# Performance work log

Measured on AMD Instinct MI355X. Metric: run time of the kernel, lower is better.

The kernel has to match this reference:

```python
import jax, jax.numpy as jnp
import numpy as np

B, T, E, H = 8, 4096, 1024, 128

def setup_inputs() -> dict:
    key = jax.random.key(0)
    kx, kq, kk, kv = jax.random.split(key, 4)
    x = jax.random.normal(kx, (B, T, E), dtype=jnp.float32)
    # bias-free Linear weights stored as (in, out) for x @ W
    scale = 1.0 / np.sqrt(E)
    Wq = jax.random.normal(kq, (E, H), dtype=jnp.float32) * scale
    Wk = jax.random.normal(kk, (E, H), dtype=jnp.float32) * scale
    Wv = jax.random.normal(kv, (E, H), dtype=jnp.float32) * scale
    return {"x": x, "Wq": Wq, "Wk": Wk, "Wv": Wv}

def reference(x, Wq, Wk, Wv):
    # x: (B,T,E) -> out: (B,T,H). Causal single-head attention, dropout p=0 (no-op).
    q = x @ Wq  # (B,T,H)
    k = x @ Wk
    v = x @ Wv
    head_norm = jnp.sqrt(jnp.float32(q.shape[-1]))
    att = jnp.einsum('bth,bsh->bts', q, k) / head_norm  # (B,T,T)
    causal = jnp.tril(jnp.ones((x.shape[1], x.shape[1]), dtype=bool))
    att = jnp.where(causal, att, -jnp.inf)
    att = jax.nn.softmax(att, axis=-1)
    return jnp.einsum('bts,bsh->bth', att, v)
```

## Files before the change

### kernel.cpp

```cpp
#include <hip/hip_runtime.h>
#include <hip/hip_bf16.h>
#include <stdint.h>

#define Bn 8
#define Tn 4096
#define En 1024
#define Hn 128
#define SCALE 0.08838834764831845f

typedef __attribute__((ext_vector_type(8))) short bf16x8;
typedef __attribute__((ext_vector_type(4))) float f32x4;

__device__ __forceinline__ float bf2f(unsigned short v) {
    return __uint_as_float(((unsigned int)v) << 16);
}
__device__ __forceinline__ unsigned int pkbf(float a, float b) {
    __hip_bfloat162 h = __float22bfloat162_rn(make_float2(a, b));
    union { __hip_bfloat162 h2; unsigned int u; } cv;
    cv.h2 = h;
    return cv.u;
}

__device__ __forceinline__ void gll16(const unsigned short* g, unsigned short* l) {
    __builtin_amdgcn_global_load_lds(
        (const __attribute__((address_space(1))) void*)g,
        (__attribute__((address_space(3))) void*)l, 16, 0, 0);
}

__global__ __launch_bounds__(256)
void xcvt(const float* __restrict__ x, unsigned short* __restrict__ xb) {
    const size_t i = ((size_t)blockIdx.x * 256 + threadIdx.x) * 16;
    const float4* src = (const float4*)(x + i);
    float4 a = src[0], b = src[1], c = src[2], d = src[3];
    uint4 o0, o1;
    o0.x = pkbf(a.x, a.y); o0.y = pkbf(a.z, a.w);
    o0.z = pkbf(b.x, b.y); o0.w = pkbf(b.z, b.w);
    o1.x = pkbf(c.x, c.y); o1.y = pkbf(c.z, c.w);
    o1.z = pkbf(d.x, d.y); o1.w = pkbf(d.z, d.w);
    *(uint4*)(xb + i) = o0;
    *(uint4*)(xb + i + 8) = o1;
}

__global__ __launch_bounds__(256)
void wcvt(const float* __restrict__ Wq, const float* __restrict__ Wk,
          const float* __restrict__ Wv, unsigned short* __restrict__ wt3) {
    const int which = blockIdx.x;
    const int k0 = blockIdx.y * 128;
    const float* W = (which == 0) ? Wq : (which == 1) ? Wk : Wv;
    unsigned short* wt = wt3 + (size_t)which * 131072;

    __shared__ unsigned short wl[128 * 132];
    const int t = threadIdx.x;
#pragma unroll
    for (int i = 0; i < 16; ++i) {
        const int idx = t + i * 256;
        const int k = idx >> 5, c4 = idx & 31;
        float4 v = *(const float4*)&W[(size_t)(k0 + k) * Hn + c4 * 4];
        uint2 p;
        p.x = pkbf(v.x, v.y);
        p.y = pkbf(v.z, v.w);
        *(uint2*)&wl[k * 132 + c4 * 4] = p;
    }
    __syncthreads();
#pragma unroll
    for (int j = 0; j < 32; ++j) {
        const int idx = t + j * 256;
        const int n = idx >> 6, kp = idx & 63;
        unsigned int u = (unsigned int)wl[(2 * kp) * 132 + n] |
                         ((unsigned int)wl[(2 * kp + 1) * 132 + n] << 16);
        *(unsigned int*)&wt[(size_t)n * 1024 + k0 + 2 * kp] = u;
    }
}

#define QSWZ(r, c) (((r) << 7) + ((c) ^ (((r) & 7) << 4)))

__global__ __launch_bounds__(256)
void qkv2(const unsigned short* __restrict__ xb,
          const unsigned short* __restrict__ wt3,
          unsigned short* __restrict__ Qo,
          unsigned short* __restrict__ Ko,
          unsigned short* __restrict__ Vo) {
    const int mt = blockIdx.x;
    const int which = blockIdx.y;
    const unsigned short* wt = wt3 + (size_t)which * 131072;
    unsigned short* out = (which == 0) ? Qo : (which == 1) ? Ko : Vo;
    const float scale = (which == 0) ? SCALE : 1.0f;

    __shared__ alignas(16) unsigned short Xs[2][128 * 64];
    __shared__ alignas(16) unsigned short Ws[2][128 * 64];

    const int t = threadIdx.x;
    const int w = t >> 6;
    const int lane = t & 63;
    const int quad = lane >> 4;
    const int l16 = lane & 15;
    const int r8 = lane >> 3;
    const int cb = lane & 7;

    const unsigned short* xtile = xb + (size_t)(mt * 128) * En;

    f32x4 acc[2][8];
#pragma unroll
    for (int mi = 0; mi < 2; ++mi)
#pragma unroll
        for (int nst = 0; nst < 8; ++nst) acc[mi][nst] = (f32x4){0.f, 0.f, 0.f, 0.f};

    auto stage = [&](int buf, int kt) {
#pragma unroll
        for (int i = 0; i < 4; ++i) {
            const int row = i * 32 + w * 8 + r8;
            gll16(xtile + (size_t)row * En + kt * 64 + ((cb ^ (row & 7)) * 8),
                  &Xs[buf][(i * 32 + w * 8) * 64]);
        }
#pragma unroll
        for (int i = 0; i < 4; ++i) {
            const int row = i * 32 + w * 8 + r8;
            gll16(wt + (size_t)row * 1024 + kt * 64 + ((cb ^ (row & 7)) * 8),
                  &Ws[buf][(i * 32 + w * 8) * 64]);
        }
    };

    stage(0, 0);
    __syncthreads();

    for (int kt = 0; kt < 16; ++kt) {
        const int buf = kt & 1;
        if (kt < 15) stage(buf ^ 1, kt + 1);
        const char* xs = (const char*)Xs[buf];
        const char* ws = (const char*)Ws[buf];
#pragma unroll
        for (int ks = 0; ks < 2; ++ks) {
            bf16x8 af[2];
#pragma unroll
            for (int mi = 0; mi < 2; ++mi)
                af[mi] = *(const bf16x8*)(xs + QSWZ(w * 32 + mi * 16 + l16, ks * 64 + quad * 16));
#pragma unroll
            for (int nst = 0; nst < 8; ++nst) {
                bf16x8 bfr = *(const bf16x8*)(ws + QSWZ(nst * 16 + l16, ks * 64 + quad * 16));
                acc[0][nst] = __builtin_amdgcn_mfma_f32_16x16x32_bf16(bfr, af[0], acc[0][nst], 0, 0, 0);
                acc[1][nst] = __builtin_amdgcn_mfma_f32_16x16x32_bf16(bfr, af[1], acc[1][nst], 0, 0, 0);
            }
        }
        if (kt < 15) __syncthreads();
    }

#pragma unroll
    for (int mi = 0; mi < 2; ++mi) {
        const size_t rowbase = (size_t)(mt * 128 + w * 32 + mi * 16 + l16) * Hn;
#pragma unroll
        for (int nst = 0; nst < 8; ++nst) {
            f32x4 v = acc[mi][nst];
            uint2 pk;
            pk.x = pkbf(v[0] * scale, v[1] * scale);
            pk.y = pkbf(v[2] * scale, v[3] * scale);
            *(uint2*)(out + rowbase + nst * 16 + quad * 4) = pk;
        }
    }
}

__global__ __launch_bounds__(256)
void qkv_mfma(const float* __restrict__ x,
              const float* __restrict__ Wq,
              const float* __restrict__ Wk,
              const float* __restrict__ Wv,
              unsigned short* __restrict__ Qo,
              unsigned short* __restrict__ Ko,
              unsigned short* __restrict__ Vo) {
    const int mt = blockIdx.x;
    const int which = blockIdx.y;
    const float* W = (which == 0) ? Wq : (which == 1) ? Wk : Wv;
    unsigned short* out = (which == 0) ? Qo : (which == 1) ? Ko : Vo;
    const float scale = (which == 0) ? SCALE : 1.0f;

    __shared__ alignas(16) unsigned short Xs[128 * 72];
    __shared__ alignas(16) unsigned short Wt[128 * 72];

    const int t = threadIdx.x;
    const int w = t >> 6;
    const int lane = t & 63;
    const int quad = lane >> 4;
    const int l16 = lane & 15;

    const int xrow = t >> 1;
    const int xkc = (t & 1) * 32;
    const int ws0 = (t & 31) * 2;
    const int wd0 = (t >> 5) * 16;

    const float* xsrc0 = x + (size_t)(mt * 128 + xrow) * En + xkc;

    f32x4 acc[2][8];
#pragma unroll
    for (int mi = 0; mi < 2; ++mi)
#pragma unroll
        for (int nst = 0; nst < 8; ++nst) acc[mi][nst] = (f32x4){0.f, 0.f, 0.f, 0.f};

    float4 xpre[8], wpre[8];
    {
        const float* src = xsrc0;
#pragma unroll
        for (int i = 0; i < 8; ++i) xpre[i] = *(const float4*)(src + i * 4);
        const float* w0 = W + (size_t)ws0 * Hn + wd0;
        const float* w1 = w0 + Hn;
#pragma unroll
        for (int i = 0; i < 4; ++i) wpre[i] = *(const float4*)(w0 + i * 4);
#pragma unroll
        for (int i = 0; i < 4; ++i) wpre[4 + i] = *(const float4*)(w1 + i * 4);
    }

    for (int kt = 0; kt < 16; ++kt) {
        __syncthreads();
        {
            unsigned int u[16];
#pragma unroll
            for (int i = 0; i < 8; ++i) {
                u[2 * i]     = pkbf(xpre[i].x, xpre[i].y);
                u[2 * i + 1] = pkbf(xpre[i].z, xpre[i].w);
            }
#pragma unroll
            for (int i = 0; i < 4; ++i)
                *(uint4*)&Xs[xrow * 72 + xkc + i * 8] = ((const uint4*)u)[i];

            const float* ax = (const float*)&wpre[0];
            const float* bx = (const float*)&wpre[4];
#pragma unroll
            for (int dd = 0; dd < 16; ++dd)
                *(unsigned int*)&Wt[(wd0 + dd) * 72 + ws0] = pkbf(ax[dd], bx[dd]);
        }
        if (kt < 15) {
            const float* src = xsrc0 + (kt + 1) * 64;
#pragma unroll
            for (int i = 0; i < 8; ++i) xpre[i] = *(const float4*)(src + i * 4);
            const float* w0 = W + (size_t)((kt + 1) * 64 + ws0) * Hn + wd0;
            const float* w1 = w0 + Hn;
#pragma unroll
            for (int i = 0; i < 4; ++i) wpre[i] = *(const float4*)(w0 + i * 4);
#pragma unroll
            for (int i = 0; i < 4; ++i) wpre[4 + i] = *(const float4*)(w1 + i * 4);
        }
        __syncthreads();

#pragma unroll
        for (int ks = 0; ks < 2; ++ks) {
            bf16x8 af[2];
#pragma unroll
            for (int mi = 0; mi < 2; ++mi)
                af[mi] = *(const bf16x8*)&Xs[(w * 32 + mi * 16 + l16) * 72 + ks * 32 + quad * 8];
#pragma unroll
            for (int nst = 0; nst < 8; ++nst) {
                bf16x8 bfr = *(const bf16x8*)&Wt[(nst * 16 + l16) * 72 + ks * 32 + quad * 8];
                acc[0][nst] = __builtin_amdgcn_mfma_f32_16x16x32_bf16(bfr, af[0], acc[0][nst], 0, 0, 0);
                acc[1][nst] = __builtin_amdgcn_mfma_f32_16x16x32_bf16(bfr, af[1], acc[1][nst], 0, 0, 0);
            }
        }
    }

#pragma unroll
    for (int mi = 0; mi < 2; ++mi) {
        const size_t rowbase = (size_t)(mt * 128 + w * 32 + mi * 16 + l16) * Hn;
#pragma unroll
        for (int nst = 0; nst < 8; ++nst) {
            f32x4 v = acc[mi][nst];
            uint2 pk;
            pk.x = pkbf(v[0] * scale, v[1] * scale);
            pk.y = pkbf(v[2] * scale, v[3] * scale);
            *(uint2*)(out + rowbase + nst * 16 + quad * 4) = pk;
        }
    }
}

#define KSWZ(r, c) (((r) << 8) + ((c) ^ (((r) & 7) << 4)))
#define VSWZ(r, c) (((r) << 7) + ((c) ^ (((r) & 7) << 4)))

__global__ __launch_bounds__(256, 2)
void flash_mfma(const unsigned short* __restrict__ Qb,
                const unsigned short* __restrict__ Kb,
                const unsigned short* __restrict__ Vb,
                float* __restrict__ out) {
    const int b = blockIdx.x;
    const int bx = blockIdx.y;
    const int qt = (bx < 32) ? (63 - bx) : (bx - 32);
    const int t = threadIdx.x;
    const int w = t >> 6;
    const int g = w >> 1;
    const int rg = w & 1;
    const int lane = t & 63;
    const int quad = lane >> 4;
    const int l16 = lane & 15;
    const int t128 = t & 127;

    extern __shared__ unsigned short pool[];
    char* const poolb = (char*)pool;
    char* const Kg = poolb + g * 16384;
    char* const Vg = poolb + 32768 + g * 16384;
    char* const Pw = poolb + 65536 + w * 4096;
    float* const Os = (float*)poolb;
    float* const Ex = (float*)(poolb + 40960);
    float* const Em = (float*)(poolb + 73728);
    float* const El = Em + 64;

    const size_t gbase = (size_t)b * ((size_t)Tn * Hn);
    const unsigned short* kbase = Kb + gbase;
    const unsigned short* vbase = Vb + gbase;

    const int l_hi = lane >> 4;
    const int cpr = (lane & 15) * 16;
    const int vs0 = (t128 & 31) * 2;
    const int vd0 = (t128 >> 5) * 32;

    uint4 va0, va1, va2, va3, vb0, vb1, vb2, vb3;
    if (g <= qt) {
        const unsigned short* vsrc = vbase + (size_t)(g * 64) * Hn;
        va0 = *(const uint4*)&vsrc[vs0 * 128 + vd0];
        va1 = *(const uint4*)&vsrc[vs0 * 128 + vd0 + 8];
        va2 = *(const uint4*)&vsrc[vs0 * 128 + vd0 + 16];
        va3 = *(const uint4*)&vsrc[vs0 * 128 + vd0 + 24];
        vb0 = *(const uint4*)&vsrc[(vs0 + 1) * 128 + vd0];
        vb1 = *(const uint4*)&vsrc[(vs0 + 1) * 128 + vd0 + 8];
        vb2 = *(const uint4*)&vsrc[(vs0 + 1) * 128 + vd0 + 16];
        vb3 = *(const uint4*)&vsrc[(vs0 + 1) * 128 + vd0 + 24];
    }

    {
        const unsigned short* qsrc = Qb + gbase + (size_t)(qt * 64) * Hn;
#pragma unroll
        for (int i = 0; i < 4; ++i) {
            const int row = w * 16 + i * 4 + l_hi;
            const int scol = cpr ^ ((row & 7) << 4);
            gll16(qsrc + row * 128 + (scol >> 1),
                  (unsigned short*)(poolb + w * 4096 + i * 1024));
        }
    }
    __syncthreads();

    bf16x8 qf[2][4];
#pragma unroll
    for (int s = 0; s < 2; ++s)
#pragma unroll
        for (int ks = 0; ks < 4; ++ks)
            qf[s][ks] = *(const bf16x8*)(poolb + KSWZ(rg * 32 + s * 16 + l16, ks * 64 + quad * 16));

    f32x4 acc_o[2][8];
#pragma unroll
    for (int s = 0; s < 2; ++s)
#pragma unroll
        for (int i = 0; i < 8; ++i) acc_o[s][i] = (f32x4){0.f, 0.f, 0.f, 0.f};
    float m_run[2] = {-1e30f, -1e30f};
    float l_run[2] = {0.f, 0.f};

    const int n = (qt >> 1) + 1;
    for (int it = 0; it < n; ++it) {
        const int kt = 2 * it + g;
        const bool active = (kt <= qt);
        __syncthreads();
        if (active) {
            const unsigned short* ktile = kbase + (size_t)(kt * 64) * Hn;
#pragma unroll
            for (int i = 0; i < 8; ++i) {
                const int row = rg * 32 + i * 4 + l_hi;
                const int scol = cpr ^ ((row & 7) << 4);
                gll16(ktile + row * 128 + (scol >> 1),
                      (unsigned short*)(Kg + rg * 8192 + i * 1024));
            }
            const unsigned short* pa0 = (const unsigned short*)&va0;
            const unsigned short* pa1 = (const unsigned short*)&va1;
            const unsigned short* pa2 = (const unsigned short*)&va2;
            const unsigned short* pa3 = (const unsigned short*)&va3;
            const unsigned short* pb0 = (const unsigned short*)&vb0;
            const unsigned short* pb1 = (const unsigned short*)&vb1;
            const unsigned short* pb2 = (const unsigned short*)&vb2;
            const unsigned short* pb3 = (const unsigned short*)&vb3;
#pragma unroll
            for (int dd = 0; dd < 8; ++dd)
                *(unsigned int*)(Vg + VSWZ(vd0 + dd, vs0 * 2)) =
                    (unsigned int)pa0[dd] | ((unsigned int)pb0[dd] << 16);
#pragma unroll
            for (int dd = 0; dd < 8; ++dd)
                *(unsigned int*)(Vg + VSWZ(vd0 + 8 + dd, vs0 * 2)) =
                    (unsigned int)pa1[dd] | ((unsigned int)pb1[dd] << 16);
#pragma unroll
            for (int dd = 0; dd < 8; ++dd)
                *(unsigned int*)(Vg + VSWZ(vd0 + 16 + dd, vs0 * 2)) =
                    (unsigned int)pa2[dd] | ((unsigned int)pb2[dd] << 16);
#pragma unroll
            for (int dd = 0; dd < 8; ++dd)
                *(unsigned int*)(Vg + VSWZ(vd0 + 24 + dd, vs0 * 2)) =
                    (unsigned int)pa3[dd] | ((unsigned int)pb3[dd] << 16);
        }
        __syncthreads();
        if (kt + 2 <= qt) {
            const unsigned short* vsrc = vbase + (size_t)((kt + 2) * 64) * Hn;
            va0 = *(const uint4*)&vsrc[vs0 * 128 + vd0];
            va1 = *(const uint4*)&vsrc[vs0 * 128 + vd0 + 8];
            va2 = *(const uint4*)&vsrc[vs0 * 128 + vd0 + 16];
            va3 = *(const uint4*)&vsrc[vs0 * 128 + vd0 + 24];
            vb0 = *(const uint4*)&vsrc[(vs0 + 1) * 128 + vd0];
            vb1 = *(const uint4*)&vsrc[(vs0 + 1) * 128 + vd0 + 8];
            vb2 = *(const uint4*)&vsrc[(vs0 + 1) * 128 + vd0 + 16];
            vb3 = *(const uint4*)&vsrc[(vs0 + 1) * 128 + vd0 + 24];
        }
        if (!active) continue;

        const bool diag = (kt == qt);
        f32x4 sa[2][4];
#pragma unroll
        for (int st = 0; st < 4; ++st) {
            const bool skipAll = diag && (st > rg * 2 + 1);
            bf16x8 kf[4];
            if (!skipAll) {
#pragma unroll
                for (int ks = 0; ks < 4; ++ks)
                    kf[ks] = *(const bf16x8*)(Kg + KSWZ(st * 16 + l16, ks * 64 + quad * 16));
            }
#pragma unroll
            for (int s = 0; s < 2; ++s) {
                const int qs = rg * 2 + s;
                if (diag && st > qs) {
                    sa[s][st] = (f32x4){-1e30f, -1e30f, -1e30f, -1e30f};
                } else {
                    f32x4 c = (f32x4){0.f, 0.f, 0.f, 0.f};
#pragma unroll
                    for (int ks = 0; ks < 4; ++ks)
                        c = __builtin_amdgcn_mfma_f32_16x16x32_bf16(kf[ks], qf[s][ks], c, 0, 0, 0);
                    if (diag && st == qs) {
#pragma unroll
                        for (int r = 0; r < 4; ++r)
                            if (quad * 4 + r > l16) c[r] = -1e30f;
                    }
                    sa[s][st] = c;
                }
            }
        }

#pragma unroll
        for (int s = 0; s < 2; ++s) {
            float mloc = -1e30f;
#pragma unroll
            for (int st = 0; st < 4; ++st)
#pragma unroll
                for (int r = 0; r < 4; ++r) mloc = fmaxf(mloc, sa[s][st][r]);
            mloc = fmaxf(mloc, __shfl_xor(mloc, 16));
            mloc = fmaxf(mloc, __shfl_xor(mloc, 32));
            const float m_new = fmaxf(m_run[s], mloc);
            const float alpha = __expf(m_run[s] - m_new);
            float lsum = 0.f;
#pragma unroll
            for (int st = 0; st < 4; ++st)
#pragma unroll
                for (int r = 0; r < 4; ++r) {
                    const float e = __expf(sa[s][st][r] - m_new);
                    sa[s][st][r] = e;
                    lsum += e;
                }
            lsum += __shfl_xor(lsum, 16);
            lsum += __shfl_xor(lsum, 32);
            l_run[s] = l_run[s] * alpha + lsum;
            m_run[s] = m_new;
#pragma unroll
            for (int i = 0; i < 8; ++i) acc_o[s][i] *= alpha;
#pragma unroll
            for (int st = 0; st < 4; ++st) {
                uint2 pk;
                pk.x = pkbf(sa[s][st][0], sa[s][st][1]);
                pk.y = pkbf(sa[s][st][2], sa[s][st][3]);
                *(uint2*)(Pw + VSWZ(s * 16 + l16, st * 32 + quad * 8)) = pk;
            }
        }
        bf16x8 pf[2][2];
#pragma unroll
        for (int s = 0; s < 2; ++s) {
            pf[s][0] = *(const bf16x8*)(Pw + VSWZ(s * 16 + l16, quad * 16));
            pf[s][1] = *(const bf16x8*)(Pw + VSWZ(s * 16 + l16, 64 + quad * 16));
        }

#pragma unroll
        for (int dt = 0; dt < 8; ++dt) {
            bf16x8 vf0 = *(const bf16x8*)(Vg + VSWZ(dt * 16 + l16, quad * 16));
            bf16x8 vf1 = *(const bf16x8*)(Vg + VSWZ(dt * 16 + l16, 64 + quad * 16));
#pragma unroll
            for (int s = 0; s < 2; ++s) {
                acc_o[s][dt] = __builtin_amdgcn_mfma_f32_16x16x32_bf16(vf0, pf[s][0], acc_o[s][dt], 0, 0, 0);
                acc_o[s][dt] = __builtin_amdgcn_mfma_f32_16x16x32_bf16(vf1, pf[s][1], acc_o[s][dt], 0, 0, 0);
            }
        }
    }

    __syncthreads();
    if (g == 1) {
#pragma unroll
        for (int s = 0; s < 2; ++s) {
            const int row = rg * 32 + s * 16 + l16;
            float* dst = Ex + row * 128;
#pragma unroll
            for (int dt = 0; dt < 8; ++dt)
                *(f32x4*)&dst[dt * 16 + quad * 4] = acc_o[s][dt];
            if (quad == 0) {
                Em[row] = m_run[s];
                El[row] = l_run[s];
            }
        }
    }
    __syncthreads();
    if (g == 0) {
#pragma unroll
        for (int s = 0; s < 2; ++s) {
            const int row = rg * 32 + s * 16 + l16;
            const float* src = Ex + row * 128;
            const float m2 = Em[row];
            const float l2 = El[row];
            const float ms = fmaxf(m_run[s], m2);
            const float a1 = __expf(m_run[s] - ms);
            const float a2 = __expf(m2 - ms);
            const float linv = 1.f / (l_run[s] * a1 + l2 * a2);
#pragma unroll
            for (int dt = 0; dt < 8; ++dt) {
                f32x4 o2 = *(const f32x4*)&src[dt * 16 + quad * 4];
                f32x4 v = (acc_o[s][dt] * a1 + o2 * a2) * linv;
                *(f32x4*)&Os[row * 132 + dt * 16 + quad * 4] = v;
            }
        }
    }
    __syncthreads();
    float* dst = out + gbase + (size_t)(qt * 64) * Hn;
#pragma unroll
    for (int i = 0; i < 8; ++i) {
        const int idx = (t + i * 256) * 4;
        const int row = idx >> 7, col = idx & 127;
        *(float4*)&dst[row * 128 + col] = *(const float4*)&Os[row * 132 + col];
    }
}

extern "C" void kernel_launch(void* const* d_in, const int* in_sizes, int n_in,
                              void* d_out, int out_size, void* d_ws, size_t ws_size,
                              hipStream_t stream) {
    const float* x  = (const float*)d_in[0];
    const float* Wq = (const float*)d_in[1];
    const float* Wk = (const float*)d_in[2];
    const float* Wv = (const float*)d_in[3];
    float* o = (float*)d_out;

    const size_t qkvb = (size_t)Bn * Tn * Hn;
    unsigned short* Qb = (unsigned short*)d_ws;
    unsigned short* Kb = Qb + qkvb;
    unsigned short* Vb = Kb + qkvb;
    unsigned short* xbf = Vb + qkvb;
    unsigned short* wt3 = xbf + (size_t)Bn * Tn * En;

    const size_t ws_need = (3 * qkvb + (size_t)Bn * Tn * En + 3 * (size_t)Hn * En)
                           * sizeof(unsigned short);

    static bool attr_done = false;
    if (!attr_done) {
        hipFuncSetAttribute((const void*)flash_mfma,
                            hipFuncAttributeMaxDynamicSharedMemorySize, 81920);
        attr_done = true;
    }

    if (ws_size >= ws_need) {
        xcvt<<<8192, 256, 0, stream>>>(x, xbf);
        wcvt<<<dim3(3, 8), 256, 0, stream>>>(Wq, Wk, Wv, wt3);
        qkv2<<<dim3(256, 3), 256, 0, stream>>>(xbf, wt3, Qb, Kb, Vb);
    } else {
        qkv_mfma<<<dim3(256, 3), 256, 0, stream>>>(x, Wq, Wk, Wv, Qb, Kb, Vb);
    }
    flash_mfma<<<dim3(8, 64), 256, 81920, stream>>>(Qb, Kb, Vb, o);
}
```

Measured before the change: 357.4 us.

## Split flash attention KV loop across four warp groups per block

The attention kernel goes from 256 to 512 threads, so four warp groups each take every fourth key tile instead of two groups taking every other one. The shared-memory pool doubles to 160KB to hold K/V tiles for four groups and three partial output buffers. The final merge now combines four online-softmax partials per row. The goal is to halve the serial key-tile iterations and barriers per block. In exchange, a block now fills a CU's LDS, more groups sit idle at the causal tail, and launch_bounds(512,2) tightens the register budget, which may cause spills.

Result: slower. 370.1 us (+3.5%).

```diff
diff --git a/kernel.cpp b/kernel.cpp
--- a/kernel.cpp
+++ b/kernel.cpp
@@ -271,7 +271,7 @@
 #define KSWZ(r, c) (((r) << 8) + ((c) ^ (((r) & 7) << 4)))
 #define VSWZ(r, c) (((r) << 7) + ((c) ^ (((r) & 7) << 4)))
 
-__global__ __launch_bounds__(256, 2)
+__global__ __launch_bounds__(512, 2)
 void flash_mfma(const unsigned short* __restrict__ Qb,
                 const unsigned short* __restrict__ Kb,
                 const unsigned short* __restrict__ Vb,
@@ -291,12 +291,12 @@
     extern __shared__ unsigned short pool[];
     char* const poolb = (char*)pool;
     char* const Kg = poolb + g * 16384;
-    char* const Vg = poolb + 32768 + g * 16384;
-    char* const Pw = poolb + 65536 + w * 4096;
-    float* const Os = (float*)poolb;
-    float* const Ex = (float*)(poolb + 40960);
-    float* const Em = (float*)(poolb + 73728);
-    float* const El = Em + 64;
+    char* const Vg = poolb + 65536 + g * 16384;
+    char* const Pw = poolb + 131072 + w * 4096;
+    float* const Ex = (float*)poolb;
+    float* const Em = (float*)(poolb + 98304);
+    float* const El = (float*)(poolb + 99072);
+    float* const Os = (float*)(poolb + 99840);
 
     const size_t gbase = (size_t)b * ((size_t)Tn * Hn);
     const unsigned short* kbase = Kb + gbase;
@@ -323,11 +323,11 @@
     {
         const unsigned short* qsrc = Qb + gbase + (size_t)(qt * 64) * Hn;
 #pragma unroll
-        for (int i = 0; i < 4; ++i) {
-            const int row = w * 16 + i * 4 + l_hi;
+        for (int i = 0; i < 2; ++i) {
+            const int row = w * 8 + i * 4 + l_hi;
             const int scol = cpr ^ ((row & 7) << 4);
             gll16(qsrc + row * 128 + (scol >> 1),
-                  (unsigned short*)(poolb + w * 4096 + i * 1024));
+                  (unsigned short*)(poolb + w * 2048 + i * 1024));
         }
     }
     __syncthreads();
@@ -347,9 +347,9 @@
     float m_run[2] = {-1e30f, -1e30f};
     float l_run[2] = {0.f, 0.f};
 
-    const int n = (qt >> 1) + 1;
-    for (int it = 0; it < n; ++it) {
-        const int kt = 2 * it + g;
+    const int nIt = (qt >> 2) + 1;
+    for (int it = 0; it < nIt; ++it) {
+        const int kt = 4 * it + g;
         const bool active = (kt <= qt);
         __syncthreads();
         if (active) {
@@ -387,8 +387,8 @@
                     (unsigned int)pa3[dd] | ((unsigned int)pb3[dd] << 16);
         }
         __syncthreads();
-        if (kt + 2 <= qt) {
-            const unsigned short* vsrc = vbase + (size_t)((kt + 2) * 64) * Hn;
+        if (kt + 4 <= qt) {
+            const unsigned short* vsrc = vbase + (size_t)((kt + 4) * 64) * Hn;
             va0 = *(const uint4*)&vsrc[vs0 * 128 + vd0];
             va1 = *(const uint4*)&vsrc[vs0 * 128 + vd0 + 8];
             va2 = *(const uint4*)&vsrc[vs0 * 128 + vd0 + 16];
@@ -485,17 +485,17 @@
     }
 
     __syncthreads();
-    if (g == 1) {
+    if (g > 0) {
 #pragma unroll
         for (int s = 0; s < 2; ++s) {
             const int row = rg * 32 + s * 16 + l16;
-            float* dst = Ex + row * 128;
+            float* dst = Ex + ((g - 1) * 64 + row) * 128;
 #pragma unroll
             for (int dt = 0; dt < 8; ++dt)
                 *(f32x4*)&dst[dt * 16 + quad * 4] = acc_o[s][dt];
             if (quad == 0) {
-                Em[row] = m_run[s];
-                El[row] = l_run[s];
+                Em[(g - 1) * 64 + row] = m_run[s];
+                El[(g - 1) * 64 + row] = l_run[s];
             }
         }
     }
@@ -504,26 +504,35 @@
 #pragma unroll
         for (int s = 0; s < 2; ++s) {
             const int row = rg * 32 + s * 16 + l16;
-            const float* src = Ex + row * 128;
-            const float m2 = Em[row];
-            const float l2 = El[row];
-            const float ms = fmaxf(m_run[s], m2);
-            const float a1 = __expf(m_run[s] - ms);
+            const float m0 = m_run[s], l0 = l_run[s];
+            const float m1 = Em[row],       l1 = El[row];
+            const float m2 = Em[64 + row],  l2 = El[64 + row];
+            const float m3 = Em[128 + row], l3 = El[128 + row];
+            const float ms = fmaxf(fmaxf(m0, m1), fmaxf(m2, m3));
+            const float a0 = __expf(m0 - ms);
+            const float a1 = __expf(m1 - ms);
             const float a2 = __expf(m2 - ms);
-            const float linv = 1.f / (l_run[s] * a1 + l2 * a2);
+            const float a3 = __expf(m3 - ms);
+            const float linv = 1.f / (a0 * l0 + a1 * l1 + a2 * l2 + a3 * l3);
+            const float* s1 = Ex + row * 128;
+            const float* s2 = Ex + (64 + row) * 128;
+            const float* s3 = Ex + (128 + row) * 128;
 #pragma unroll
             for (int dt = 0; dt < 8; ++dt) {
-                f32x4 o2 = *(const f32x4*)&src[dt * 16 + quad * 4];
-                f32x4 v = (acc_o[s][dt] * a1 + o2 * a2) * linv;
-                *(f32x4*)&Os[row * 132 + dt * 16 + quad * 4] = v;
+                const int c = dt * 16 + quad * 4;
+                f32x4 v = acc_o[s][dt] * a0;
+                v += (*(const f32x4*)&s1[c]) * a1;
+                v += (*(const f32x4*)&s2[c]) * a2;
+                v += (*(const f32x4*)&s3[c]) * a3;
+                *(f32x4*)&Os[row * 132 + c] = v * linv;
             }
         }
     }
     __syncthreads();
     float* dst = out + gbase + (size_t)(qt * 64) * Hn;
 #pragma unroll
-    for (int i = 0; i < 8; ++i) {
-        const int idx = (t + i * 256) * 4;
+    for (int i = 0; i < 4; ++i) {
+        const int idx = (t + i * 512) * 4;
         const int row = idx >> 7, col = idx & 127;
         *(float4*)&dst[row * 128 + col] = *(const float4*)&Os[row * 132 + col];
     }
@@ -551,7 +560,7 @@
     static bool attr_done = false;
     if (!attr_done) {
         hipFuncSetAttribute((const void*)flash_mfma,
-                            hipFuncAttributeMaxDynamicSharedMemorySize, 81920);
+                            hipFuncAttributeMaxDynamicSharedMemorySize, 163840);
         attr_done = true;
     }
 
@@ -562,5 +571,5 @@
     } else {
         qkv_mfma<<<dim3(256, 3), 256, 0, stream>>>(x, Wq, Wk, Wv, Qb, Kb, Vb);
     }
-    flash_mfma<<<dim3(8, 64), 256, 81920, stream>>>(Qb, Kb, Vb, o);
-}
+    flash_mfma<<<dim3(8, 64), 512, 163840, stream>>>(Qb, Kb, Vb, o);
+}
```
